# Kernel optimization log

Measured on AMD Instinct MI355X. Metric: run time of the kernel, lower is better.

The kernel has to match this reference:

```python
import jax, jax.numpy as jnp
from jax import lax
import numpy as np

B, T, D = 16, 4096, 512          # batch, encoder length, d_model
C, FW = 10, 100                  # aconv_chans, aconv_filts (kernel width 2*FW+1)
SHARP = 2.0                      # sharpening_factor


def setup_inputs() -> dict:
    key = jax.random.key(0)
    ks = jax.random.split(key, 11)
    s = 1.0 / np.sqrt(D)
    sc = 1.0 / np.sqrt(2 * FW + 1)
    return {
        "value": jax.random.normal(ks[0], (B, T, D), jnp.float32),
        "query": jax.random.normal(ks[1], (B, D), jnp.float32),
        "input_lengths": jax.random.randint(ks[2], (B,), T // 2, T + 1),
        "att_prev": jax.random.uniform(ks[3], (B, T), jnp.float32),
        # learned parameters (torch Linear stores W as [out,in]; y = x @ W.T + b)
        "W_enc": jax.random.uniform(ks[4], (D, D), jnp.float32, -s, s),
        "b_enc": jax.random.uniform(ks[5], (D,), jnp.float32, -s, s),
        "W_dec": jax.random.uniform(ks[6], (D, D), jnp.float32, -s, s),
        "W_att": jax.random.uniform(ks[7], (D, C), jnp.float32, -s, s),
        "W_conv": jax.random.uniform(ks[8], (C, 1, 2 * FW + 1), jnp.float32, -sc, sc),
        "w_g": jax.random.uniform(ks[9], (1, D), jnp.float32, -s, s),
        "b_g": jax.random.uniform(ks[10], (1,), jnp.float32, -s, s),
    }


def reference(value, query, input_lengths, att_prev,
              W_enc, b_enc, W_dec, W_att, W_conv, w_g, b_g):
    # pre_compute_enc_h = mlp_enc(enc_h): [B,T,D]
    pre_enc = jnp.einsum('btd,ed->bte', value, W_enc) + b_enc
    # dec_z_tiled = mlp_dec(dec_z): [B,1,D]
    dec_tiled = (query @ W_dec.T)[:, None, :]
    # loc_conv: 1D conv over T, in_ch=1 -> out_ch=C, same padding -> [B,C,T]
    conv = lax.conv_general_dilated(att_prev[:, None, :], W_conv,
                                    window_strides=(1,), padding=[(FW, FW)],
                                    dimension_numbers=('NCH', 'OIH', 'NCH'))
    # mlp_att on transposed conv: [B,T,C] @ W_att.T -> [B,T,D]
    att_conv = jnp.einsum('bct,dc->btd', conv, W_att)
    # e = gvec(tanh(sum)): [B,T]
    e = jnp.einsum('btd,d->bt', jnp.tanh(att_conv + pre_enc + dec_tiled), w_g[0]) + b_g[0]
    # pad mask: positions >= length are masked to -inf (use large finite neg)
    pad_mask = jnp.arange(T)[None, :] >= input_lengths[:, None]
    e = jnp.where(pad_mask, -1e30, e)
    att_weights = jax.nn.softmax(SHARP * e, axis=1)            # [B,T]
    context = jnp.einsum('btd,bt->bd', value, att_weights)     # [B,D]
    return context, att_weights
```

## Files before the change

kernel.cpp:

```cpp
#include <hip/hip_runtime.h>
#include <hip/hip_bf16.h>

constexpr int kB  = 16;
constexpr int kT  = 4096;
constexpr int kD  = 512;
constexpr int kC  = 10;
constexpr int kFW = 100;
constexpr int kKW = 2 * kFW + 1;
constexpr int kKP = 576;

typedef __attribute__((ext_vector_type(8))) short short8_t;
typedef __attribute__((ext_vector_type(4))) float float4_t;

__device__ __forceinline__ float tanh_fast(float x) {
  float ax = fabsf(x);
  float z  = __expf(-2.0f * ax);
  float r  = (1.0f - z) / (1.0f + z);
  return copysignf(r, x);
}

__device__ __forceinline__ short f2bf(float x) {
  unsigned u = __float_as_uint(x);
  u += 0x7fffu + ((u >> 16) & 1u);
  return (short)(u >> 16);
}

__device__ __forceinline__ unsigned pk2(float lo, float hi) {
  __hip_bfloat162 h = __float22bfloat162_rn(make_float2(lo, hi));
  union { __hip_bfloat162 h2; unsigned u; } cv; cv.h2 = h; return cv.u;
}

__device__ __forceinline__ float bf2f(short s) {
  return __uint_as_float(((unsigned)(unsigned short)s) << 16);
}

__device__ __forceinline__ void glds16(const void* g, void* l) {
  __builtin_amdgcn_global_load_lds(
      (const __attribute__((address_space(1))) void*)g,
      (__attribute__((address_space(3))) void*)l, 16, 0, 0);
}

__global__ __launch_bounds__(256) void prep_kernel(
    const float* __restrict__ query, const float* __restrict__ W_dec,
    const float* __restrict__ b_enc, float* __restrict__ bias,
    const float* __restrict__ W_enc, const float* __restrict__ W_att,
    short* __restrict__ Wbf,
    const float* __restrict__ att_prev, const float* __restrict__ W_conv,
    const float* __restrict__ value, const int* __restrict__ lens,
    short* __restrict__ Abf) {
  __shared__ float ap[256 + 2 * kFW];
  __shared__ float wc[kC * kKW];
  int blk = blockIdx.x;
  int tid = threadIdx.x;

  if (blk < 2048) {
    int gw   = (blk * 256 + tid) >> 6;
    int lane = tid & 63;
    int b = gw >> 9, d = gw & (kD - 1);
    const float* q = query + (size_t)b * kD;
    const float* w = W_dec + (size_t)d * kD;
    float s = 0.f;
#pragma unroll
    for (int k0 = 0; k0 < kD; k0 += 256) {
      float4 qa = *(const float4*)(q + k0 + lane * 4);
      float4 wa = *(const float4*)(w + k0 + lane * 4);
      s += qa.x * wa.x + qa.y * wa.y + qa.z * wa.z + qa.w * wa.w;
    }
#pragma unroll
    for (int off = 32; off > 0; off >>= 1) s += __shfl_down(s, off, 64);
    if (lane == 0) bias[gw] = b_enc[d] + s;
  } else if (blk < 2048 + 512) {
    int d = blk - 2048;
    for (int c = tid; c < kKP; c += 256) {
      float v = 0.f;
      if (c < kD)           v = W_enc[(size_t)d * kD + c];
      else if (c < kD + kC) v = W_att[(size_t)d * kC + (c - kD)];
      Wbf[(size_t)d * kKP + c] = f2bf(v);
    }
  } else if (blk < 2048 + 512 + 256) {
    int lin = blk - 2560;
    int b = lin >> 4, t0 = (lin & 15) * 256;
    for (int i = tid; i < kC * kKW; i += 256) wc[i] = W_conv[i];
    for (int i = tid; i < 256 + 2 * kFW; i += 256) {
      int p = t0 - kFW + i;
      ap[i] = (p >= 0 && p < kT) ? att_prev[(size_t)b * kT + p] : 0.f;
    }
    __syncthreads();
    float acc[kC];
#pragma unroll
    for (int c = 0; c < kC; ++c) acc[c] = 0.f;
    for (int j = 0; j < kKW; ++j) {
      float a = ap[tid + j];
#pragma unroll
      for (int c = 0; c < kC; ++c) acc[c] += a * wc[c * kKW + j];
    }
    unsigned ow[32];
#pragma unroll
    for (int i = 0; i < 5; ++i) ow[i] = pk2(acc[2 * i], acc[2 * i + 1]);
#pragma unroll
    for (int i = 5; i < 32; ++i) ow[i] = 0u;
    uint4* out = (uint4*)(Abf + ((size_t)b * kT + t0 + tid) * kKP + kD);
#pragma unroll
    for (int i = 0; i < 8; ++i)
      out[i] = make_uint4(ow[4 * i], ow[4 * i + 1], ow[4 * i + 2], ow[4 * i + 3]);
  } else {
    int lin = blk - 2816;
    int b = lin >> 6, t0 = (lin & 63) * 64;
    if (t0 >= lens[b]) return;
    const float* src = value + ((size_t)b * kT + t0) * kD;
    short* dst = Abf + ((size_t)b * kT + t0) * kKP;
#pragma unroll
    for (int i = 0; i < 16; ++i) {
      int c = tid + i * 256;
      int row = c >> 6, col = (c & 63) * 8;
      float4 f0 = *(const float4*)(src + (size_t)row * kD + col);
      float4 f1 = *(const float4*)(src + (size_t)row * kD + col + 4);
      uint4 o;
      o.x = pk2(f0.x, f0.y); o.y = pk2(f0.z, f0.w);
      o.z = pk2(f1.x, f1.y); o.w = pk2(f1.z, f1.w);
      *(uint4*)(dst + (size_t)row * kKP + col) = o;
    }
  }
}

__global__ __launch_bounds__(256) void e_kernel(
    const short* __restrict__ Abf, const short* __restrict__ Wbf,
    const float* __restrict__ bias, const float* __restrict__ w_g,
    const int* __restrict__ lens, float* __restrict__ e_part) {
  __shared__ short As[128 * 64];
  __shared__ short Bs[128 * 64];

  int tid = threadIdx.x;
  int L    = blockIdx.x;
  int xcd  = L & 7;
  int slot = L >> 3;
  int bn   = slot & 3;
  int mt   = (slot >> 2) * 8 + xcd;
  int b  = mt >> 5;
  int t0 = (mt & 31) * 128;
  if (t0 >= lens[b]) return;
  int n0 = bn * 128;

  int w    = tid >> 6;
  int lane = tid & 63;
  int nl   = lane & 15;
  int quad = lane >> 4;
  int wm = w >> 1, wn = w & 1;

  int r8 = lane >> 3;
  int kc = (lane & 7) ^ r8;
  const short* asrc = Abf + ((size_t)(b * kT + t0) + w * 32 + r8) * kKP + kc * 8;
  const short* bsrc = Wbf + (size_t)(n0 + w * 32 + r8) * kKP + kc * 8;
  short* adst = &As[(w * 32) * 64];
  short* bdst = &Bs[(w * 32) * 64];

  int axr = nl & 7;
  const short* aBase = &As[(wm * 64 + nl) * 64];
  const short* bBase = &Bs[(wn * 64 + nl) * 64];
  int co0 = ((0 * 4 + quad) ^ axr) * 8;
  int co1 = ((1 * 4 + quad) ^ axr) * 8;

  float4_t acc[4][4] = {};

  for (int kk = 0; kk < 9; ++kk) {
    int ko = kk * 64;
    __syncthreads();
#pragma unroll
    for (int j = 0; j < 4; ++j) {
      glds16(asrc + ko + (size_t)(j * 8) * kKP, adst + j * 8 * 64);
      glds16(bsrc + ko + (size_t)(j * 8) * kKP, bdst + j * 8 * 64);
    }
    __syncthreads();
#pragma unroll
    for (int ks = 0; ks < 2; ++ks) {
      int co = ks ? co1 : co0;
      short8_t a_frag[4], b_frag[4];
#pragma unroll
      for (int i = 0; i < 4; ++i) a_frag[i] = *(const short8_t*)(aBase + i * 1024 + co);
#pragma unroll
      for (int j = 0; j < 4; ++j) b_frag[j] = *(const short8_t*)(bBase + j * 1024 + co);
#pragma unroll
      for (int i = 0; i < 4; ++i)
#pragma unroll
        for (int j = 0; j < 4; ++j)
          acc[i][j] = __builtin_amdgcn_mfma_f32_16x16x32_bf16(
              a_frag[i], b_frag[j], acc[i][j], 0, 0, 0);
    }
  }

  float bias_r[4], wg_r[4];
#pragma unroll
  for (int j = 0; j < 4; ++j) {
    int d = n0 + wn * 64 + j * 16 + nl;
    bias_r[j] = bias[b * kD + d];
    wg_r[j]   = w_g[d];
  }
  int p = wn * 4 + bn;
  float* ep = e_part + ((size_t)p * kB + b) * kT + t0 + wm * 64;
#pragma unroll
  for (int i = 0; i < 4; ++i) {
#pragma unroll
    for (int r = 0; r < 4; ++r) {
      float s = 0.f;
#pragma unroll
      for (int j = 0; j < 4; ++j)
        s += wg_r[j] * tanh_fast(acc[i][j][r] + bias_r[j]);
      s += __shfl_xor(s, 1, 64);
      s += __shfl_xor(s, 2, 64);
      s += __shfl_xor(s, 4, 64);
      s += __shfl_xor(s, 8, 64);
      if (nl == 0) ep[i * 16 + quad * 4 + r] = s;
    }
  }
}

__global__ void softmax1_kernel(const float* __restrict__ e_part,
                                const int* __restrict__ lens,
                                float* __restrict__ eb,
                                float* __restrict__ stats) {
  __shared__ float sred[256];
  int b = blockIdx.x >> 3, ch = blockIdx.x & 7;
  int tid = threadIdx.x;
  int len = lens[b];
  int base = ch * 512;
  const float* ep = e_part + (size_t)b * kT + base;
  float v[2];
  float m = -3.0e38f;
#pragma unroll
  for (int i = 0; i < 2; ++i) {
    int t = tid + i * 256;
    if (base + t < len) {
      float s = 0.f;
#pragma unroll
      for (int p = 0; p < 8; ++p) s += ep[(size_t)p * kB * kT + t];
      eb[(size_t)b * kT + base + t] = s;
      v[i] = s;
      m = fmaxf(m, s);
    } else {
      v[i] = -3.0e38f;
    }
  }
  sred[tid] = m; __syncthreads();
  for (int s = 128; s > 0; s >>= 1) {
    if (tid < s) sred[tid] = fmaxf(sred[tid], sred[tid + s]);
    __syncthreads();
  }
  m = sred[0]; __syncthreads();
  float l = 0.f;
#pragma unroll
  for (int i = 0; i < 2; ++i)
    if (v[i] > -1.0e38f) l += __expf(2.0f * (v[i] - m));
  sred[tid] = l; __syncthreads();
  for (int s = 128; s > 0; s >>= 1) {
    if (tid < s) sred[tid] += sred[tid + s];
    __syncthreads();
  }
  if (tid == 0) {
    stats[(b * 8 + ch) * 2]     = m;
    stats[(b * 8 + ch) * 2 + 1] = sred[0];
  }
}

__global__ void softmax2_kernel(const float* __restrict__ eb,
                                const float* __restrict__ stats,
                                const int* __restrict__ lens,
                                float* __restrict__ att,
                                float* __restrict__ ctx) {
  int b = blockIdx.x, tid = threadIdx.x;
  int len = lens[b];
  ctx[b * kD + tid * 2]     = 0.f;
  ctx[b * kD + tid * 2 + 1] = 0.f;
  float M = -3.0e38f;
#pragma unroll
  for (int p = 0; p < 8; ++p) M = fmaxf(M, stats[(b * 8 + p) * 2]);
  float L = 0.f;
#pragma unroll
  for (int p = 0; p < 8; ++p) {
    float mc = stats[(b * 8 + p) * 2], lc = stats[(b * 8 + p) * 2 + 1];
    if (lc > 0.f) L += lc * __expf(2.0f * (mc - M));
  }
  float inv = 1.0f / L;
  const float* e = eb + (size_t)b * kT;
  float* a = att + (size_t)b * kT;
#pragma unroll
  for (int i = 0; i < 16; ++i) {
    int t = tid + i * 256;
    a[t] = (t < len) ? __expf(2.0f * (e[t] - M)) * inv : 0.0f;
  }
}

__global__ void context_kernel(const short* __restrict__ Abf,
                               const float* __restrict__ att,
                               const int* __restrict__ lens,
                               float* __restrict__ ctx) {
  __shared__ float red[4][kD];
  int b = blockIdx.y;
  int len = lens[b];
  int t0 = blockIdx.x * 128;
  if (t0 >= len) return;
  int w = threadIdx.x >> 6, lane = threadIdx.x & 63;
  int tb = t0 + w * 32;
  int tmax = min(32, len - tb);
  float a[8] = {0.f, 0.f, 0.f, 0.f, 0.f, 0.f, 0.f, 0.f};
  const short* vp = Abf + ((size_t)b * kT + tb) * kKP + lane * 8;
  const float* ap = att + (size_t)b * kT + tb;
  for (int t = 0; t < tmax; ++t) {
    float wt = ap[t];
    short8_t v = *(const short8_t*)(vp + (size_t)t * kKP);
#pragma unroll
    for (int i = 0; i < 8; ++i) a[i] += wt * bf2f(v[i]);
  }
#pragma unroll
  for (int i = 0; i < 8; ++i) red[w][lane * 8 + i] = a[i];
  __syncthreads();
  int tid = threadIdx.x;
  for (int col = tid; col < kD; col += 256) {
    float s = red[0][col] + red[1][col] + red[2][col] + red[3][col];
    atomicAdd(&ctx[b * kD + col], s);
  }
}

extern "C" void kernel_launch(void* const* d_in, const int* in_sizes, int n_in,
                              void* d_out, int out_size, void* d_ws, size_t ws_size,
                              hipStream_t stream) {
  const float* value    = (const float*)d_in[0];
  const float* query    = (const float*)d_in[1];
  const int*   lens     = (const int*)  d_in[2];
  const float* att_prev = (const float*)d_in[3];
  const float* W_enc    = (const float*)d_in[4];
  const float* b_enc    = (const float*)d_in[5];
  const float* W_dec    = (const float*)d_in[6];
  const float* W_att    = (const float*)d_in[7];
  const float* W_conv   = (const float*)d_in[8];
  const float* w_g      = (const float*)d_in[9];

  float* ws     = (float*)d_ws;
  float* e_part = ws;
  float* eb     = e_part + (size_t)8 * kB * kT;
  float* stats  = eb + (size_t)kB * kT;
  float* bias   = stats + 256;
  short* Wbf    = (short*)(bias + (size_t)kB * kD);
  short* Abf    = Wbf + (size_t)kD * kKP;
  float* ctx = (float*)d_out;
  float* att = ctx + (size_t)kB * kD;

  prep_kernel<<<3840, 256, 0, stream>>>(query, W_dec, b_enc, bias,
                                        W_enc, W_att, Wbf,
                                        att_prev, W_conv, value, lens, Abf);
  e_kernel<<<2048, 256, 0, stream>>>(Abf, Wbf, bias, w_g, lens, e_part);
  softmax1_kernel<<<kB * 8, 256, 0, stream>>>(e_part, lens, eb, stats);
  softmax2_kernel<<<kB, 256, 0, stream>>>(eb, stats, lens, att, (float*)d_out);
  context_kernel<<<dim3(kT / 128, kB), 256, 0, stream>>>(Abf, att, lens, ctx);
}
```

Before: 295.6 us.

## Shrink K padding to 544, fuse softmax normalization into context kernel

Reduces the padded K dimension of the packed bf16 activation/weight matrix from 576 to 544, so the GEMM runs 8 full K-tiles plus a half-width 32-wide tail tile instead of 9 full tiles, and the prep kernel writes less padding. The second softmax pass and the context kernel are merged into one kernel that recomputes attention weights from the logits and per-chunk stats while accumulating the context. Context zeroing moves into the first softmax kernel. This removes one launch and a global round-trip of attention weights and cuts wasted MFMA work and memory traffic, at the cost of a more complex tail-tile load with its own swizzle and an occupancy hint on the GEMM.

New measurement: 295.1 us. No clear change (-0.2%).

```diff
diff --git a/kernel.cpp b/kernel.cpp
--- a/kernel.cpp
+++ b/kernel.cpp
@@ -7,7 +7,7 @@
 constexpr int kC  = 10;
 constexpr int kFW = 100;
 constexpr int kKW = 2 * kFW + 1;
-constexpr int kKP = 576;
+constexpr int kKP = 544;
 
 typedef __attribute__((ext_vector_type(8))) short short8_t;
 typedef __attribute__((ext_vector_type(4))) float float4_t;
@@ -94,14 +94,14 @@
 #pragma unroll
       for (int c = 0; c < kC; ++c) acc[c] += a * wc[c * kKW + j];
     }
-    unsigned ow[32];
+    unsigned ow[16];
 #pragma unroll
     for (int i = 0; i < 5; ++i) ow[i] = pk2(acc[2 * i], acc[2 * i + 1]);
 #pragma unroll
-    for (int i = 5; i < 32; ++i) ow[i] = 0u;
+    for (int i = 5; i < 16; ++i) ow[i] = 0u;
     uint4* out = (uint4*)(Abf + ((size_t)b * kT + t0 + tid) * kKP + kD);
 #pragma unroll
-    for (int i = 0; i < 8; ++i)
+    for (int i = 0; i < 4; ++i)
       out[i] = make_uint4(ow[4 * i], ow[4 * i + 1], ow[4 * i + 2], ow[4 * i + 3]);
   } else {
     int lin = blk - 2816;
@@ -123,7 +123,7 @@
   }
 }
 
-__global__ __launch_bounds__(256) void e_kernel(
+__global__ __launch_bounds__(256, 4) void e_kernel(
     const short* __restrict__ Abf, const short* __restrict__ Wbf,
     const float* __restrict__ bias, const float* __restrict__ w_g,
     const int* __restrict__ lens, float* __restrict__ e_part) {
@@ -162,7 +162,7 @@
 
   float4_t acc[4][4] = {};
 
-  for (int kk = 0; kk < 9; ++kk) {
+  for (int kk = 0; kk < 8; ++kk) {
     int ko = kk * 64;
     __syncthreads();
 #pragma unroll
@@ -186,6 +186,35 @@
           acc[i][j] = __builtin_amdgcn_mfma_f32_16x16x32_bf16(
               a_frag[i], b_frag[j], acc[i][j], 0, 0, 0);
     }
+  }
+
+  {
+    __syncthreads();
+    int r4  = lane >> 2;
+    int kc4 = (lane & 3) ^ (r4 & 3);
+    const short* asrcT = Abf + ((size_t)(b * kT + t0) + w * 32 + r4) * kKP + 512 + kc4 * 8;
+    const short* bsrcT = Wbf + (size_t)(n0 + w * 32 + r4) * kKP + 512 + kc4 * 8;
+    short* adstT = &As[(w * 32) * 32];
+    short* bdstT = &Bs[(w * 32) * 32];
+    glds16(asrcT,                adstT);
+    glds16(asrcT + 16 * kKP,     adstT + 16 * 32);
+    glds16(bsrcT,                bdstT);
+    glds16(bsrcT + 16 * kKP,     bdstT + 16 * 32);
+    __syncthreads();
+    int coT = (quad ^ (nl & 3)) * 8;
+    const short* aBT = &As[(wm * 64 + nl) * 32];
+    const short* bBT = &Bs[(wn * 64 + nl) * 32];
+    short8_t a_frag[4], b_frag[4];
+#pragma unroll
+    for (int i = 0; i < 4; ++i) a_frag[i] = *(const short8_t*)(aBT + i * 512 + coT);
+#pragma unroll
+    for (int j = 0; j < 4; ++j) b_frag[j] = *(const short8_t*)(bBT + j * 512 + coT);
+#pragma unroll
+    for (int i = 0; i < 4; ++i)
+#pragma unroll
+      for (int j = 0; j < 4; ++j)
+        acc[i][j] = __builtin_amdgcn_mfma_f32_16x16x32_bf16(
+            a_frag[i], b_frag[j], acc[i][j], 0, 0, 0);
   }
 
   float bias_r[4], wg_r[4];
@@ -217,11 +246,16 @@
 __global__ void softmax1_kernel(const float* __restrict__ e_part,
                                 const int* __restrict__ lens,
                                 float* __restrict__ eb,
-                                float* __restrict__ stats) {
+                                float* __restrict__ stats,
+                                float* __restrict__ ctx) {
   __shared__ float sred[256];
   int b = blockIdx.x >> 3, ch = blockIdx.x & 7;
   int tid = threadIdx.x;
   int len = lens[b];
+  if (ch == 0) {
+    ctx[b * kD + tid]       = 0.f;
+    ctx[b * kD + 256 + tid] = 0.f;
+  }
   int base = ch * 512;
   const float* ep = e_part + (size_t)b * kT + base;
   float v[2];
@@ -261,51 +295,40 @@
   }
 }
 
-__global__ void softmax2_kernel(const float* __restrict__ eb,
-                                const float* __restrict__ stats,
-                                const int* __restrict__ lens,
-                                float* __restrict__ att,
-                                float* __restrict__ ctx) {
-  int b = blockIdx.x, tid = threadIdx.x;
-  int len = lens[b];
-  ctx[b * kD + tid * 2]     = 0.f;
-  ctx[b * kD + tid * 2 + 1] = 0.f;
-  float M = -3.0e38f;
-#pragma unroll
-  for (int p = 0; p < 8; ++p) M = fmaxf(M, stats[(b * 8 + p) * 2]);
-  float L = 0.f;
-#pragma unroll
-  for (int p = 0; p < 8; ++p) {
-    float mc = stats[(b * 8 + p) * 2], lc = stats[(b * 8 + p) * 2 + 1];
-    if (lc > 0.f) L += lc * __expf(2.0f * (mc - M));
-  }
-  float inv = 1.0f / L;
-  const float* e = eb + (size_t)b * kT;
-  float* a = att + (size_t)b * kT;
-#pragma unroll
-  for (int i = 0; i < 16; ++i) {
-    int t = tid + i * 256;
-    a[t] = (t < len) ? __expf(2.0f * (e[t] - M)) * inv : 0.0f;
-  }
-}
-
-__global__ void context_kernel(const short* __restrict__ Abf,
-                               const float* __restrict__ att,
+__global__ void ctx_att_kernel(const float* __restrict__ eb,
+                               const float* __restrict__ stats,
                                const int* __restrict__ lens,
+                               const short* __restrict__ Abf,
+                               float* __restrict__ att,
                                float* __restrict__ ctx) {
   __shared__ float red[4][kD];
   int b = blockIdx.y;
   int len = lens[b];
   int t0 = blockIdx.x * 128;
+  int tid = threadIdx.x;
+  float M = -3.0e38f;
+#pragma unroll
+  for (int p = 0; p < 8; ++p) M = fmaxf(M, stats[(b * 8 + p) * 2]);
+  float Lsum = 0.f;
+#pragma unroll
+  for (int p = 0; p < 8; ++p) {
+    float mc = stats[(b * 8 + p) * 2], lc = stats[(b * 8 + p) * 2 + 1];
+    if (lc > 0.f) Lsum += lc * __expf(2.0f * (mc - M));
+  }
+  float inv = 1.0f / Lsum;
+  const float* e = eb + (size_t)b * kT + t0;
+  if (tid < 128) {
+    int t = t0 + tid;
+    att[(size_t)b * kT + t] = (t < len) ? __expf(2.0f * (e[tid] - M)) * inv : 0.0f;
+  }
   if (t0 >= len) return;
-  int w = threadIdx.x >> 6, lane = threadIdx.x & 63;
-  int tb = t0 + w * 32;
-  int tmax = min(32, len - tb);
+  int w = tid >> 6, lane = tid & 63;
+  int tb = w * 32;
+  int tmax = min(32, len - t0 - tb);
   float a[8] = {0.f, 0.f, 0.f, 0.f, 0.f, 0.f, 0.f, 0.f};
-  const short* vp = Abf + ((size_t)b * kT + tb) * kKP + lane * 8;
-  const float* ap = att + (size_t)b * kT + tb;
+  const short* vp = Abf + ((size_t)b * kT + t0 + tb) * kKP + lane * 8;
   for (int t = 0; t < tmax; ++t) {
-    float wt = ap[t];
+    float wt = __expf(2.0f * (e[tb + t] - M)) * inv;
     short8_t v = *(const short8_t*)(vp + (size_t)t * kKP);
 #pragma unroll
     for (int i = 0; i < 8; ++i) a[i] += wt * bf2f(v[i]);
@@ -313,7 +336,6 @@
 #pragma unroll
   for (int i = 0; i < 8; ++i) red[w][lane * 8 + i] = a[i];
   __syncthreads();
-  int tid = threadIdx.x;
   for (int col = tid; col < kD; col += 256) {
     float s = red[0][col] + red[1][col] + red[2][col] + red[3][col];
     atomicAdd(&ctx[b * kD + col], s);
@@ -348,7 +370,6 @@
                                         W_enc, W_att, Wbf,
                                         att_prev, W_conv, value, lens, Abf);
   e_kernel<<<2048, 256, 0, stream>>>(Abf, Wbf, bias, w_g, lens, e_part);
-  softmax1_kernel<<<kB * 8, 256, 0, stream>>>(e_part, lens, eb, stats);
-  softmax2_kernel<<<kB, 256, 0, stream>>>(eb, stats, lens, att, (float*)d_out);
-  context_kernel<<<dim3(kT / 128, kB), 256, 0, stream>>>(Abf, att, lens, ctx);
-}
+  softmax1_kernel<<<kB * 8, 256, 0, stream>>>(e_part, lens, eb, stats, ctx);
+  ctx_att_kernel<<<dim3(kT / 128, kB), 256, 0, stream>>>(eb, stats, lens, Abf, att, ctx);
+}
```
